# Kernel tuning notes

Hardware: AMD Instinct MI355X
Metric: run time of the kernel (lower is better)

The kernel has to match this reference:

```python
import jax, jax.numpy as jnp
import numpy as np

B, C_IN, C_OUT, N, T = 32, 64, 192, 307, 24
DILATIONS = (1, 2)
O3 = C_OUT // 3  # out channels per branch


def setup_inputs() -> dict:
    key = jax.random.key(0)
    ks = iter(jax.random.split(key, 32))
    nrm = lambda shape: 0.05 * jax.random.normal(next(ks), shape, dtype=jnp.float32)
    return {
        "x": jax.random.normal(next(ks), (B, C_IN, N, T), dtype=jnp.float32),
        "adj": jax.random.randint(next(ks), (N, N), 0, 2, dtype=jnp.int32),
        "ln_g": jnp.ones((T,), jnp.float32),
        "ln_b": jnp.zeros((T,), jnp.float32),
        "res_W": nrm((C_OUT, C_IN)), "res_b": nrm((C_OUT,)),
        "ca_W1": nrm((T,)), "ca_W2": nrm((N, T)), "ca_W3": nrm((N,)),
        "cc_W": nrm((O3, C_IN)), "cc_b": nrm((O3,)),
        "ta_W1": nrm((N,)), "ta_W2": nrm((C_IN, N)), "ta_W3": nrm((C_IN,)),
        "tc_W0": nrm((O3, C_IN, 1, 2)), "tc_b0": nrm((O3,)),
        "tc_W1": nrm((O3, O3, 1, 2)), "tc_b1": nrm((O3,)),
        "ga_W1": nrm((T,)), "ga_W2": nrm((C_IN, T)), "ga_W3": nrm((C_IN,)),
        "g_W": nrm((O3, C_IN)),
    }


def layer_norm_lastdim(x, g, b, eps=1e-5):
    mu = jnp.mean(x, axis=-1, keepdims=True)
    var = jnp.var(x, axis=-1, keepdims=True)
    return (x - mu) * jax.lax.rsqrt(var + eps) * g + b


def conv1x1(x, W, b):
    # x: [B,C,N,T], W: [O,C]
    return jnp.einsum("oc,bcnt->bont", W, x) + b[None, :, None, None]


def c_attention(x, W1, W2, W3):
    # channel attention over C; x: [B,C,N,T]
    lhs = jnp.einsum("bcn,nt->bct", jnp.einsum("bcnt,t->bcn", x, W1), W2)  # [B,C,T]
    rhs = jnp.einsum("n,bcnt->bct", W3, x)                                  # [B,C,T]
    att = jax.nn.softmax(jnp.einsum("bct,bdt->bcd", lhs, rhs), axis=-1)     # [B,C,C]
    return jnp.einsum("bcd,bdnt->bcnt", att, x)


def t_attention(x, W1, W2, W3):
    # temporal attention over T; x: [B,C,N,T]
    lhs = jnp.einsum("bct,cn->btn", jnp.einsum("bcnt,n->bct", x, W1), W2)   # [B,T,N]
    rhs = jnp.einsum("c,bcnt->bnt", W3, x)                                   # [B,N,T]
    att = jax.nn.softmax(jnp.einsum("btn,bns->bts", lhs, rhs), axis=-1)      # [B,T,T]
    return jnp.einsum("bts,bcns->bcnt", att, x)


def g_attention(x, adj, W1, W2, W3):
    # graph (spatial) attention over N, masked by adjacency; x: [B,C,N,T]
    lhs = jnp.einsum("bcn,ct->bnt", jnp.einsum("bcnt,t->bcn", x, W1), W2)   # [B,N,T]
    rhs = jnp.einsum("c,bcnt->bnt", W3, x)                                   # [B,N,T]
    scores = jnp.einsum("bnt,bmt->bnm", lhs, rhs)                            # [B,N,N]
    scores = jnp.where(adj[None] > 0, scores, jnp.float32(-1e30))
    att = jax.nn.softmax(scores, axis=-1)
    return jnp.einsum("bnm,bcmt->bcnt", att, x)


def causal_conv(x, W, b, d):
    # Conv2d kernel [1,2], dilation [1,d], pad [0,d] + Chomp(d) == left-pad-only causal conv
    y = jax.lax.conv_general_dilated(
        x, W, window_strides=(1, 1), padding=((0, 0), (d, 0)),
        rhs_dilation=(1, d), dimension_numbers=("NCHW", "OIHW", "NCHW"))
    return y + b[None, :, None, None]


def meam_forward(x, adj, ln_g, ln_b, res_W, res_b, ca_W1, ca_W2, ca_W3, cc_W, cc_b,
                 ta_W1, ta_W2, ta_W3, tc_W0, tc_b0, tc_W1, tc_b1,
                 ga_W1, ga_W2, ga_W3, g_W):
    h = layer_norm_lastdim(x, ln_g, ln_b)
    # CACN branch: channel attention + 1x1 conv
    c_out = conv1x1(c_attention(h, ca_W1, ca_W2, ca_W3), cc_W, cc_b)
    # TACN branch: temporal attention + dilated causal convs
    t_out = t_attention(h, ta_W1, ta_W2, ta_W3)
    t_out = causal_conv(t_out, tc_W0, tc_b0, DILATIONS[0])
    t_out = causal_conv(t_out, tc_W1, tc_b1, DILATIONS[1])
    # GACN branch: graph attention + channel mixing
    g_out = jnp.einsum("oc,bcnt->bont", g_W, g_attention(h, adj, ga_W1, ga_W2, ga_W3))
    out = jnp.concatenate([c_out, t_out, g_out], axis=1)  # [B, C_OUT, N, T]
    return jax.nn.relu(out + conv1x1(x, res_W, res_b))


def reference(x, adj, ln_g, ln_b, res_W, res_b, ca_W1, ca_W2, ca_W3, cc_W, cc_b,
              ta_W1, ta_W2, ta_W3, tc_W0, tc_b0, tc_W1, tc_b1,
              ga_W1, ga_W2, ga_W3, g_W):
    return meam_forward(x, adj, ln_g, ln_b, res_W, res_b, ca_W1, ca_W2, ca_W3, cc_W, cc_b,
                        ta_W1, ta_W2, ta_W3, tc_W0, tc_b0, tc_W1, tc_b1,
                        ga_W1, ga_W2, ga_W3, g_W)
```

## Files before the change

### kernel.cpp

```cpp
#include <hip/hip_runtime.h>
#include <hip/hip_bf16.h>

#define BB 32
#define CC 64
#define NN 307
#define TT 24
#define CO 192
#define NT (NN*TT)
#define GO 1536

using bf16 = __hip_bfloat16;
typedef __attribute__((ext_vector_type(8))) short bf16x8;
typedef __attribute__((ext_vector_type(4))) float f32x4;

#define OFF_ln_g   0
#define OFF_ln_b   24
#define OFF_res_W  48
#define OFF_res_b  12336
#define OFF_ca_W1  12528
#define OFF_ca_W2  12552
#define OFF_ca_W3  19920
#define OFF_cc_W   20227
#define OFF_cc_b   24323
#define OFF_ta_W1  24387
#define OFF_ta_W2  24694
#define OFF_ta_W3  44342
#define OFF_tc_W0  44406
#define OFF_tc_b0  52598
#define OFF_tc_W1  52662
#define OFF_tc_b1  60854
#define OFF_ga_W1  60918
#define OFF_ga_W2  60942
#define OFF_ga_W3  62478
#define OFF_g_W    62542
#define W_TOTAL    66638

__device__ __forceinline__ float xload(const void* p, size_t i, int f) {
  return f ? ((const float*)p)[i] : __bfloat162float(((const bf16*)p)[i]);
}
__device__ __forceinline__ void ostore(void* p, size_t i, float v, int f) {
  if (f) ((float*)p)[i] = v; else ((bf16*)p)[i] = __float2bfloat16(v);
}
__device__ __forceinline__ float oload(const void* p, size_t i, int f) {
  return f ? ((const float*)p)[i] : __bfloat162float(((const bf16*)p)[i]);
}

__global__ void MEAM_44787918963464_kernel() {}

__global__ __launch_bounds__(256) void k_probe(const void* lng_raw, int* flag) {
  if (threadIdx.x == 0 && blockIdx.x == 0) {
    unsigned w = *(const unsigned*)lng_raw;
    *flag = (w == 0x3F800000u) ? 1 : 0;
  }
}

__global__ __launch_bounds__(256) void k_cvt_w(
    const void* p0, const void* p1, const void* p2, const void* p3,
    const void* p4, const void* p5, const void* p6, const void* p7,
    const void* p8, const void* p9, const void* p10, const void* p11,
    const void* p12, const void* p13, const void* p14, const void* p15,
    const void* p16, const void* p17, const void* p18, const void* p19,
    const int* flagp, float* dst) {
  int i = blockIdx.x*256 + threadIdx.x;
  if (i >= W_TOTAL) return;
  const void* ps[20] = {p0,p1,p2,p3,p4,p5,p6,p7,p8,p9,p10,p11,p12,p13,p14,p15,p16,p17,p18,p19};
  const int sz[20] = {24,24,12288,192,24,7368,307,4096,64,307,19648,64,8192,64,8192,64,24,1536,64,4096};
  int f = *flagp;
  int s = 0, base = 0;
  while (i >= base + sz[s]) { base += sz[s]; s++; }
  dst[i] = f ? ((const float*)ps[s])[i-base]
             : __bfloat162float(((const bf16*)ps[s])[i-base]);
}

__global__ __launch_bounds__(256) void k_prep_tc(const float* __restrict__ W,
    bf16* __restrict__ Ag, float* __restrict__ tb_bias) {
  int g = blockIdx.x*256 + threadIdx.x;
  if (g >= CC*CC) return;
  int pI = g >> 6, c = g & 63;
  const float* W0 = W + OFF_tc_W0;
  const float* b0 = W + OFF_tc_b0;
  const float* W1 = W + OFF_tc_W1;
  const float* b1 = W + OFF_tc_b1;
  const float* resW = W + OFF_res_W;
  const float* resb = W + OFF_res_b;
  float m0=0.f,m1=0.f,m2=0.f,m3=0.f, bb0=0.f, bb2=0.f;
  for (int o=0;o<CC;o++){
    float a1v = W1[(pI*CC+o)*2], b1v = W1[(pI*CC+o)*2+1];
    float a0v = W0[(o*CC+c)*2],  b0v = W0[(o*CC+c)*2+1];
    m0 += b1v*b0v; m1 += b1v*a0v; m2 += a1v*b0v; m3 += a1v*a0v;
    bb0 += b1v*b0[o]; bb2 += a1v*b0[o];
  }
  Ag[pI*320 + 0*64 + c] = __float2bfloat16(m0);
  Ag[pI*320 + 1*64 + c] = __float2bfloat16(m1);
  Ag[pI*320 + 2*64 + c] = __float2bfloat16(m2);
  Ag[pI*320 + 3*64 + c] = __float2bfloat16(m3);
  Ag[pI*320 + 4*64 + c] = __float2bfloat16(resW[(64+pI)*CC + c]);
  if (c == 0){
    tb_bias[pI]    = b1[pI] + bb0 + resb[64+pI];
    tb_bias[64+pI] = bb2;
  }
}

__global__ __launch_bounds__(256) void k_prep_A(const float* __restrict__ Mc,
    const float* __restrict__ W, bf16* __restrict__ Apre) {
  int idx = blockIdx.x*256 + threadIdx.x;
  if (idx >= BB*192*128) return;
  int b = idx / 24576;
  int rem = idx - b*24576;
  int p2 = rem >> 7, k = rem & 127;
  const float* resW = W + OFF_res_W;
  const float* gW   = W + OFF_g_W;
  float v;
  if (p2 < 64)       v = (k < 64) ? Mc[b*CC*CC + p2*CC + k] : resW[p2*CC + (k-64)];
  else if (p2 < 128) v = (k < 64) ? gW[(p2-64)*CC + k] : 0.f;
  else               v = (k < 64) ? 0.f : resW[p2*CC + (k-64)];
  Apre[idx] = __float2bfloat16(v);
}

__global__ __launch_bounds__(256) void k_ln(const void* __restrict__ x, const int* flagp,
    const float* __restrict__ W,
    float* __restrict__ mu_o, float* __restrict__ rs_o,
    float* __restrict__ xw1c, float* __restrict__ xw1g) {
  int r = blockIdx.x*256 + threadIdx.x;
  if (r >= BB*CC*NN) return;
  int f = *flagp;
  const float* lng  = W + OFF_ln_g;
  const float* lnb  = W + OFF_ln_b;
  const float* caW1 = W + OFF_ca_W1;
  const float* gaW1 = W + OFF_ga_W1;
  float v[TT];
  float mu = 0.f;
  for (int t=0;t<TT;t++){ v[t] = xload(x, (size_t)r*TT+t, f); mu += v[t]; }
  mu *= (1.f/TT);
  float var = 0.f;
  for (int t=0;t<TT;t++){ float d=v[t]-mu; var += d*d; }
  var *= (1.f/TT);
  float rs = rsqrtf(var + 1e-5f);
  float s1=0.f, s2=0.f;
  for (int t=0;t<TT;t++){
    float hv = (v[t]-mu)*rs*lng[t] + lnb[t];
    s1 += hv*caW1[t];
    s2 += hv*gaW1[t];
  }
  mu_o[r]=mu; rs_o[r]=rs; xw1c[r]=s1; xw1g[r]=s2;
}

__global__ __launch_bounds__(256) void k_prep_ct(const void* __restrict__ x, const int* flagp,
    const float* __restrict__ mu_a, const float* __restrict__ rs_a,
    const float* __restrict__ W, const float* __restrict__ xw1c,
    float* __restrict__ lhsc, float* __restrict__ rhsc, float* __restrict__ xw1t) {
  int i = blockIdx.x*256 + threadIdx.x;
  if (i >= BB*CC*TT) return;
  int f = *flagp;
  const float* lng  = W + OFF_ln_g;
  const float* lnb  = W + OFF_ln_b;
  const float* caW2 = W + OFF_ca_W2;
  const float* caW3 = W + OFF_ca_W3;
  const float* taW1 = W + OFF_ta_W1;
  int t = i % TT; int bc = i / TT;
  float gt = lng[t], bt = lnb[t];
  float l=0.f, rr=0.f, xt=0.f;
  for (int n=0;n<NN;n++){
    int row = bc*NN + n;
    float hv = (xload(x, (size_t)row*TT+t, f) - mu_a[row]) * rs_a[row] * gt + bt;
    l  += xw1c[row]*caW2[n*TT+t];
    rr += caW3[n]*hv;
    xt += taW1[n]*hv;
  }
  lhsc[i]=l; rhsc[i]=rr; xw1t[i]=xt;
}

__global__ __launch_bounds__(256) void k_prep_bn(const void* __restrict__ x, const int* flagp,
    const float* __restrict__ mu_a, const float* __restrict__ rs_a,
    const float* __restrict__ W, const float* __restrict__ xw1g,
    float* __restrict__ rhst, float* __restrict__ rhsg, float* __restrict__ lhsg) {
  int i = blockIdx.x*256 + threadIdx.x;
  if (i >= BB*NN*TT) return;
  int f = *flagp;
  const float* lng  = W + OFF_ln_g;
  const float* lnb  = W + OFF_ln_b;
  const float* taW3 = W + OFF_ta_W3;
  const float* gaW3 = W + OFF_ga_W3;
  const float* gaW2 = W + OFF_ga_W2;
  int t = i % TT; int n = (i/TT)%NN; int b = i/(NN*TT);
  float gt = lng[t], bt = lnb[t];
  float a=0.f,c2=0.f,d=0.f;
  for (int c=0;c<CC;c++){
    int row = (b*CC+c)*NN + n;
    float hv = (xload(x, (size_t)row*TT+t, f) - mu_a[row]) * rs_a[row] * gt + bt;
    a  += taW3[c]*hv;
    c2 += gaW3[c]*hv;
    d  += xw1g[row]*gaW2[c*TT+t];
  }
  rhst[i]=a; rhsg[i]=c2; lhsg[i]=d;
}

__global__ __launch_bounds__(256) void k_lhs_t(const float* __restrict__ xw1t,
    const float* __restrict__ W, float* __restrict__ lhst) {
  int i = blockIdx.x*256 + threadIdx.x;
  if (i >= BB*TT*NN) return;
  const float* taW2 = W + OFF_ta_W2;
  int n = i % NN; int t = (i/NN)%TT; int b = i/(TT*NN);
  float acc=0.f;
  for (int c=0;c<CC;c++)
    acc += xw1t[(b*CC+c)*TT+t]*taW2[c*NN+n];
  lhst[i]=acc;
}

__global__ __launch_bounds__(256) void k_att_c(const float* __restrict__ lhsc,
    const float* __restrict__ rhsc, const float* __restrict__ W,
    float* __restrict__ Mc) {
  int b = blockIdx.x; int tid = threadIdx.x;
  const float* ccW = W + OFF_cc_W;
  __shared__ float lc[CC*TT], rc[CC*TT], sc[CC*(CC+1)];
  for (int e=tid;e<CC*TT;e+=256){
    lc[e]=lhsc[b*CC*TT+e];
    rc[e]=rhsc[b*CC*TT+e];
  }
  __syncthreads();
  for (int e=tid;e<CC*CC;e+=256){
    int c=e>>6, d=e&63; float s=0.f;
    for (int t=0;t<TT;t++) s += lc[c*TT+t]*rc[d*TT+t];
    sc[c*(CC+1)+d]=s;
  }
  __syncthreads();
  if (tid<CC){
    float mx=-1e30f;
    for (int d=0;d<CC;d++) mx=fmaxf(mx, sc[tid*(CC+1)+d]);
    float sum=0.f;
    for (int d=0;d<CC;d++){ float e2=__expf(sc[tid*(CC+1)+d]-mx); sc[tid*(CC+1)+d]=e2; sum+=e2; }
    float inv=1.f/sum;
    for (int d=0;d<CC;d++) sc[tid*(CC+1)+d]*=inv;
  }
  __syncthreads();
  for (int e=tid;e<CC*CC;e+=256){
    int o=e>>6, d=e&63; float acc=0.f;
    for (int c=0;c<CC;c++) acc += ccW[o*CC+c]*sc[c*(CC+1)+d];
    Mc[b*CC*CC+e]=acc;
  }
}

__global__ __launch_bounds__(256) void k_att_t(const float* __restrict__ lhst,
    const float* __restrict__ rhst, float* __restrict__ attt) {
  int b=blockIdx.x, tid=threadIdx.x;
  __shared__ float sc[TT*TT];
  for (int e=tid;e<TT*TT;e+=256){
    int t=e/TT, s=e%TT;
    float acc=0.f;
    for (int n=0;n<NN;n++)
      acc += lhst[(b*TT+t)*NN+n]*rhst[(b*NN+n)*TT+s];
    sc[e]=acc;
  }
  __syncthreads();
  if (tid < TT){
    float mx=-1e30f;
    for (int s=0;s<TT;s++) mx=fmaxf(mx,sc[tid*TT+s]);
    float sum=0.f;
    for (int s=0;s<TT;s++){ float e=__expf(sc[tid*TT+s]-mx); sc[tid*TT+s]=e; sum+=e; }
    float inv=1.f/sum;
    for (int s=0;s<TT;s++) attt[b*TT*TT + tid*TT + s]=sc[tid*TT+s]*inv;
  }
}

__global__ __launch_bounds__(256) void k_att_g(const float* __restrict__ lhsg,
    const float* __restrict__ rhsg, const int* __restrict__ adj,
    bf16* __restrict__ attgh) {
  int n = blockIdx.x, b = blockIdx.y, tid = threadIdx.x;
  __shared__ float ls[TT];
  __shared__ float sv[NN];
  __shared__ float red[256];
  if (tid < TT) ls[tid] = lhsg[(b*NN+n)*TT + tid];
  __syncthreads();
  float lmax = -1e30f;
  for (int m=tid;m<NN;m+=256){
    float s = -1e30f;
    if (adj[n*NN+m] > 0){
      const float* rr = rhsg + ((size_t)b*NN+m)*TT;
      float acc=0.f;
      for (int t=0;t<TT;t++) acc += ls[t]*rr[t];
      s = acc;
    }
    sv[m]=s; lmax=fmaxf(lmax,s);
  }
  red[tid]=lmax; __syncthreads();
  for (int k=128;k>0;k>>=1){ if (tid<k) red[tid]=fmaxf(red[tid],red[tid+k]); __syncthreads(); }
  float mx = red[0]; __syncthreads();
  float lsum=0.f;
  for (int m=tid;m<NN;m+=256){
    float e = (sv[m] > -1e29f) ? __expf(sv[m]-mx) : 0.f;
    sv[m]=e; lsum+=e;
  }
  red[tid]=lsum; __syncthreads();
  for (int k=128;k>0;k>>=1){ if (tid<k) red[tid]+=red[tid+k]; __syncthreads(); }
  float inv = 1.f/red[0];
  for (int m=tid;m<NN;m+=256)
    attgh[((size_t)b*NN+n)*NN+m] = __float2bfloat16(sv[m]*inv);
}

__global__ __launch_bounds__(256) void k_hgc_mfma(
    const void* __restrict__ x, const int* flagp,
    const float* __restrict__ mu_a, const float* __restrict__ rs_a,
    const float* __restrict__ W, const bf16* __restrict__ Apre,
    bf16* __restrict__ hg, void* __restrict__ out) {
  int jt = blockIdx.x, b = blockIdx.y, tid = threadIdx.x;
  int f = *flagp;
  int j0 = jt*64;
  const float* lng = W + OFF_ln_g;
  const float* lnb = W + OFF_ln_b;
  const float* ccb = W + OFF_cc_b;
  const float* resb= W + OFF_res_b;
  __shared__ unsigned short Bs[64*128];

  {
    int c = tid >> 2, jg = tid & 3;
    float xv[16];
    int jbase = j0 + jg*16;
    size_t xoff = (size_t)(b*CC + c)*NT + jbase;
    if (jbase + 15 < NT) {
      if (f) {
        const float4* xp = (const float4*)((const float*)x + xoff);
        #pragma unroll
        for (int v=0; v<4; v++){ float4 q = xp[v]; xv[v*4]=q.x; xv[v*4+1]=q.y; xv[v*4+2]=q.z; xv[v*4+3]=q.w; }
      } else {
        const uint4* xp = (const uint4*)((const unsigned short*)x + xoff);
        #pragma unroll
        for (int v=0; v<2; v++){
          uint4 q = xp[v]; unsigned u[4]={q.x,q.y,q.z,q.w};
          #pragma unroll
          for (int kk2=0;kk2<4;kk2++){
            union{unsigned uu;float fl;} lo,hi;
            lo.uu=u[kk2]<<16; hi.uu=u[kk2]&0xffff0000u;
            xv[v*8+kk2*2]=lo.fl; xv[v*8+kk2*2+1]=hi.fl;
          }
        }
      }
    } else {
      #pragma unroll
      for (int i=0;i<16;i++){ int j=jbase+i; xv[i] = (j<NT)? xload(x, xoff+i, f) : 0.f; }
    }
    const float* mu_r = mu_a + (b*CC+c)*NN;
    const float* rs_r = rs_a + (b*CC+c)*NN;
    #pragma unroll
    for (int i=0;i<16;i++){
      int j = jbase + i;
      int jl = jg*16 + i;
      float hv = 0.f, xf = 0.f;
      if (j < NT){
        int n = j / 24, t = j - n*24;
        xf = xv[i];
        hv = (xf - mu_r[n]) * rs_r[n] * lng[t] + lnb[t];
      }
      int cs = c ^ ((jl&7)<<3);
      bf16 hb = __float2bfloat16(hv), xb = __float2bfloat16(xf);
      Bs[jl*128 + cs]      = *(unsigned short*)&hb;
      Bs[jl*128 + cs + 64] = *(unsigned short*)&xb;
    }
  }

  int lane = tid & 63, w = tid >> 6;
  int q = lane >> 4, lr = lane & 15;
  bf16x8 afo[4], afh[2], afr[2];
  {
    const unsigned short* Ab = (const unsigned short*)Apre + (size_t)b*24576;
    const unsigned short* r0 = Ab + (w*16 + lr)*128;
    #pragma unroll
    for (int kc=0;kc<4;kc++) afo[kc] = *(const bf16x8*)&r0[kc*32 + q*8];
    const unsigned short* r1 = Ab + (64 + w*16 + lr)*128;
    #pragma unroll
    for (int kc=0;kc<2;kc++) afh[kc] = *(const bf16x8*)&r1[kc*32 + q*8];
    const unsigned short* r2 = Ab + (128 + w*16 + lr)*128;
    #pragma unroll
    for (int kc=0;kc<2;kc++) afr[kc] = *(const bf16x8*)&r2[(kc+2)*32 + q*8];
  }
  f32x4 z4 = {0.f,0.f,0.f,0.f};
  f32x4 acco[4] = {z4,z4,z4,z4};
  f32x4 acch[4] = {z4,z4,z4,z4};
  f32x4 accr[4] = {z4,z4,z4,z4};
  __syncthreads();

  #pragma unroll
  for (int ct=0; ct<4; ct++){
    int jl = ct*16 + lr;
    int sw = ((jl&7)<<3);
    #pragma unroll
    for (int kc=0; kc<4; kc++){
      int ke = (kc*32 + q*8) ^ sw;
      bf16x8 bfr = *(const bf16x8*)&Bs[jl*128 + ke];
      acco[ct] = __builtin_amdgcn_mfma_f32_16x16x32_bf16(afo[kc], bfr, acco[ct], 0,0,0);
      if (kc < 2)
        acch[ct] = __builtin_amdgcn_mfma_f32_16x16x32_bf16(afh[kc], bfr, acch[ct], 0,0,0);
      else
        accr[ct] = __builtin_amdgcn_mfma_f32_16x16x32_bf16(afr[kc-2], bfr, accr[ct], 0,0,0);
    }
  }

  #pragma unroll
  for (int ct=0;ct<4;ct++){
    int jl = ct*16 + lr;
    int j = j0 + jl;
    if (j < NT){
      #pragma unroll
      for (int r=0;r<4;r++){
        int p2 = w*16 + q*4 + r;
        float v = acco[ct][r] + ccb[p2] + resb[p2];
        ostore(out, ((size_t)b*CO + p2)*NT + j, fmaxf(v,0.f), f);
      }
      int n = j/24, t2 = j - n*24;
      size_t hb2 = ((size_t)b*NN + n)*GO + t2;
      #pragma unroll
      for (int r=0;r<4;r++){
        int o = w*16 + q*4 + r;
        hg[hb2 + o*TT] = __float2bfloat16(acch[ct][r]);
      }
      #pragma unroll
      for (int r=0;r<4;r++){
        int p3 = w*16 + q*4 + r;
        ostore(out, ((size_t)b*CO + 128 + p3)*NT + j, accr[ct][r] + resb[128+p3], f);
      }
    }
  }
}

__global__ __launch_bounds__(256) void k_gemm_g(const bf16* __restrict__ attgh,
    const bf16* __restrict__ hg, const int* flagp, void* __restrict__ out) {
  int jt = blockIdx.x, nt = blockIdx.y, b = blockIdx.z;
  int tid = threadIdx.x;
  int f = *flagp;
  int n0 = nt*64, j0 = jt*64;
  __shared__ unsigned short As[64*72];
  __shared__ unsigned short Bs[64*72];
  int lane = tid & 63, w = tid >> 6;
  int q = lane >> 4, lr = lane & 15;
  f32x4 z4 = {0.f,0.f,0.f,0.f};
  f32x4 acc[4] = {z4,z4,z4,z4};
  const unsigned short* Ag = (const unsigned short*)attgh + (size_t)b*NN*NN;
  const unsigned short* Bg = (const unsigned short*)hg + (size_t)b*NN*GO;
  for (int m0=0;m0<NN;m0+=64){
    for (int u=tid; u<512; u+=256){
      int r=u>>3, kb=(u&7)*8;
      int gn=n0+r, gm=m0+kb;
      if (gn<NN && gm+7<NN){
        *(uint4*)&As[r*72+kb] = *(const uint4*)&Ag[(size_t)gn*NN + gm];
      } else {
        for (int i2=0;i2<8;i2++){
          int m=gm+i2;
          As[r*72+kb+i2] = (gn<NN && m<NN) ? Ag[(size_t)gn*NN+m] : 0;
        }
      }
    }
    for (int u=tid; u<512; u+=256){
      int m=u>>3, jb=(u&7)*8;
      int gm=m0+m;
      if (gm<NN){
        unsigned short s[8];
        *(uint4*)s = *(const uint4*)&Bg[(size_t)gm*GO + j0 + jb];
        #pragma unroll
        for (int i2=0;i2<8;i2++) Bs[(jb+i2)*72 + m] = s[i2];
      } else {
        #pragma unroll
        for (int i2=0;i2<8;i2++) Bs[(jb+i2)*72 + m] = 0;
      }
    }
    __syncthreads();
    #pragma unroll
    for (int kk=0;kk<64;kk+=32){
      bf16x8 af = *(const bf16x8*)&As[(w*16+lr)*72 + kk + q*8];
      #pragma unroll
      for (int ct=0;ct<4;ct++){
        bf16x8 bfr = *(const bf16x8*)&Bs[(ct*16+lr)*72 + kk + q*8];
        acc[ct] = __builtin_amdgcn_mfma_f32_16x16x32_bf16(af, bfr, acc[ct], 0,0,0);
      }
    }
    __syncthreads();
  }
  #pragma unroll
  for (int ct=0;ct<4;ct++){
    #pragma unroll
    for (int r=0;r<4;r++){
      int n = n0 + w*16 + q*4 + r;
      if (n >= NN) continue;
      int j = j0 + ct*16 + lr;
      int o = j/TT, t2 = j%TT;
      size_t idx = ((size_t)b*CO + 128 + o)*NT + (size_t)n*TT + t2;
      float v = acc[ct][r] + oload(out, idx, f);
      ostore(out, idx, fmaxf(v, 0.f), f);
    }
  }
}

__global__ __launch_bounds__(256) void k_cmix(const float* __restrict__ Mc,
    const void* __restrict__ x, const int* flagp,
    const float* __restrict__ mu_a, const float* __restrict__ rs_a,
    const float* __restrict__ W, void* __restrict__ out) {
  int jt=blockIdx.x, b=blockIdx.y, tid=threadIdx.x;
  int f = *flagp;
  int j0=jt*64;
  const float* lng = W + OFF_ln_g;
  const float* lnb = W + OFF_ln_b;
  const float* ccb = W + OFF_cc_b;
  __shared__ float Ms[CC*64];
  __shared__ float Hs[CC*64];
  for (int e=tid;e<CC*64;e+=256){
    int o=e&63, d=e>>6;
    Ms[e]=Mc[b*CC*CC + o*CC + d];
  }
  for (int e=tid;e<CC*64;e+=256){
    int d=e>>6, j=e&63; int jj=j0+j;
    float hv = 0.f;
    if (jj<NT){
      int n = jj/TT, t = jj%TT;
      int row = (b*CC+d)*NN + n;
      hv = (xload(x, (size_t)(b*CC+d)*NT + jj, f) - mu_a[row]) * rs_a[row] * lng[t] + lnb[t];
    }
    Hs[e]=hv;
  }
  __syncthreads();
  int ti=tid&15, tj=tid>>4;
  float acc[4][4]={};
  for (int d=0;d<CC;d++){
    float4 a4=*(const float4*)&Ms[d*64+ti*4];
    float4 b4=*(const float4*)&Hs[d*64+tj*4];
    float av[4]={a4.x,a4.y,a4.z,a4.w};
    float bv[4]={b4.x,b4.y,b4.z,b4.w};
    for (int i=0;i<4;i++)
      for (int j=0;j<4;j++) acc[i][j]+=av[i]*bv[j];
  }
  for (int i=0;i<4;i++){
    int o=ti*4+i; float bias=ccb[o];
    for (int j=0;j<4;j++){
      int jj=j0+tj*4+j;
      if (jj<NT)
        ostore(out, ((size_t)b*CO+o)*NT+jj, acc[i][j]+bias, f);
    }
  }
}

__global__ __launch_bounds__(256) void k_graph(const float* __restrict__ lhsg,
    const float* __restrict__ rhsg, const int* __restrict__ adj,
    const void* __restrict__ x, const int* flagp,
    const float* __restrict__ mu_a, const float* __restrict__ rs_a,
    const float* __restrict__ W, void* __restrict__ out) {
  int n = blockIdx.x, b = blockIdx.y, tid = threadIdx.x;
  int f = *flagp;
  const float* lng = W + OFF_ln_g;
  const float* lnb = W + OFF_ln_b;
  const float* gW  = W + OFF_g_W;
  __shared__ float ls[TT];
  __shared__ float sv[NN];
  __shared__ float red[256];
  __shared__ float wl[NN];
  __shared__ int   ml[NN];
  __shared__ int   cnt;
  __shared__ float z[CC*TT];
  __shared__ float Gs[CC*CC];
  __shared__ float gs[TT], bs[TT];
  if (tid < TT){
    ls[tid] = lhsg[(b*NN+n)*TT + tid];
    gs[tid] = lng[tid]; bs[tid] = lnb[tid];
  }
  for (int e=tid;e<CC*CC;e+=256) Gs[e]=gW[e];
  __syncthreads();
  float lmax = -1e30f;
  for (int m=tid;m<NN;m+=256){
    float s = -1e30f;
    if (adj[n*NN+m] > 0){
      const float* rr = rhsg + ((size_t)b*NN+m)*TT;
      float acc=0.f;
      for (int t=0;t<TT;t++) acc += ls[t]*rr[t];
      s = acc;
    }
    sv[m]=s; lmax=fmaxf(lmax,s);
  }
  red[tid]=lmax; __syncthreads();
  for (int k=128;k>0;k>>=1){ if (tid<k) red[tid]=fmaxf(red[tid],red[tid+k]); __syncthreads(); }
  float mx = red[0]; __syncthreads();
  float lsum=0.f;
  for (int m=tid;m<NN;m+=256){
    float e = (sv[m] > -1e29f) ? __expf(sv[m]-mx) : 0.f;
    sv[m]=e; lsum+=e;
  }
  red[tid]=lsum; __syncthreads();
  for (int k=128;k>0;k>>=1){ if (tid<k) red[tid]+=red[tid+k]; __syncthreads(); }
  float inv = 1.f/red[0];
  if (tid==0){
    int c=0;
    for (int m=0;m<NN;m++) if (sv[m]!=0.f){ ml[c]=m; wl[c]=sv[m]*inv; c++; }
    cnt=c;
  }
  __syncthreads();
  int K = cnt;
  {
    int c = tid>>2, tg = tid&3;
    float acc[6]={0,0,0,0,0,0};
    float s0 = 0.f;
    const float* mu_r = mu_a + (b*CC+c)*NN;
    const float* rs_r = rs_a + (b*CC+c)*NN;
    size_t xbase = (size_t)(b*CC+c)*NT;
    for (int k=0;k<K;k++){
      int m = ml[k];
      float wr = wl[k]*rs_r[m];
      s0 += wr*mu_r[m];
      size_t xm = xbase + m*TT + tg*6;
      for (int j=0;j<6;j++) acc[j] += wr*xload(x, xm+j, f);
    }
    for (int j=0;j<6;j++){
      int t = tg*6+j;
      z[c*TT+t] = gs[t]*(acc[j]-s0) + bs[t];
    }
  }
  __syncthreads();
  {
    int o = tid>>2, tg = tid&3;
    float acc[6]={0,0,0,0,0,0};
    for (int c=0;c<CC;c++){
      float gwv = Gs[o*CC+c];
      const float* zr = &z[c*TT + tg*6];
      for (int j=0;j<6;j++) acc[j] += gwv*zr[j];
    }
    size_t base = ((size_t)b*CO + 128 + o)*NT + n*TT + tg*6;
    for (int j=0;j<6;j++)
      ostore(out, base+j, acc[j], f);
  }
}

__global__ __launch_bounds__(256) void k_tbranch(const void* __restrict__ x, const int* flagp,
    const float* __restrict__ mu_a, const float* __restrict__ rs_a,
    const float* __restrict__ W, const float* __restrict__ attt,
    void* __restrict__ out, int fuse) {
  int chunk = blockIdx.x, b = blockIdx.y, tid = threadIdx.x;
  int f = *flagp;
  int n0 = chunk*4;
  const float* lng = W + OFF_ln_g;
  const float* lnb = W + OFF_ln_b;
  const float* W0  = W + OFF_tc_W0;
  const float* b0  = W + OFF_tc_b0;
  const float* W1  = W + OFF_tc_W1;
  const float* b1  = W + OFF_tc_b1;
  __shared__ float hs[256*25];
  __shared__ float at[TT*TT];
  for (int e=tid;e<CC*4*TT;e+=256){
    int c=e/(4*TT), rem=e%(4*TT), i=rem/TT, t=rem%TT;
    int n=n0+i;
    float hv=0.f;
    if (n<NN){
      int row=(b*CC+c)*NN+n;
      hv = (xload(x,(size_t)row*TT+t,f) - mu_a[row]) * rs_a[row] * lng[t] + lnb[t];
    }
    hs[(c*4+i)*25+t] = hv;
  }
  for (int e=tid;e<TT*TT;e+=256) at[e]=attt[b*TT*TT+e];
  __syncthreads();
  {
    float r[TT], o2[TT];
    float* myrow = &hs[tid*25];
    #pragma unroll
    for (int s=0;s<TT;s++) r[s]=myrow[s];
    for (int t=0;t<TT;t++){
      float a=0.f;
      #pragma unroll
      for (int s=0;s<TT;s++) a += at[t*TT+s]*r[s];
      o2[t]=a;
    }
    #pragma unroll
    for (int t=0;t<TT;t++) myrow[t]=o2[t];
  }
  __syncthreads();
  {
    int o = tid>>2, i = tid&3;
    float acc[TT];
    float bb = b0[o];
    for (int t=0;t<TT;t++) acc[t]=bb;
    for (int c=0;c<CC;c++){
      float wa = W0[(o*CC+c)*2], wb = W0[(o*CC+c)*2+1];
      const float* row = &hs[(c*4+i)*25];
      acc[0] += wb*row[0];
      #pragma unroll
      for (int t=1;t<TT;t++) acc[t] += wa*row[t-1] + wb*row[t];
    }
    __syncthreads();
    float* myrow = &hs[tid*25];
    #pragma unroll
    for (int t=0;t<TT;t++) myrow[t]=acc[t];
  }
  __syncthreads();
  {
    int o2 = tid>>2, i = tid&3;
    int n = n0+i;
    float acc[TT];
    float bb = b1[o2];
    for (int t=0;t<TT;t++) acc[t]=bb;
    for (int o=0;o<CC;o++){
      float wa = W1[(o2*CC+o)*2], wb = W1[(o2*CC+o)*2+1];
      const float* row = &hs[(o*4+i)*25];
      acc[0] += wb*row[0];
      acc[1] += wb*row[1];
      #pragma unroll
      for (int t=2;t<TT;t++) acc[t] += wa*row[t-2] + wb*row[t];
    }
    if (n<NN){
      size_t base = (((size_t)b*CO + 64 + o2)*NN + n)*TT;
      if (fuse){
        for (int t=0;t<TT;t++){
          float v = acc[t] + oload(out, base+t, f);
          ostore(out, base+t, fmaxf(v,0.f), f);
        }
      } else {
        for (int t=0;t<TT;t++) ostore(out, base+t, acc[t], f);
      }
    }
  }
}

__device__ __forceinline__ void tb_load_raw(const void* __restrict__ x, int f, int b, int c, int nn,
    float* h) {
  if (nn < NN) {
    size_t off = (size_t)(b*CC + c)*NT + (size_t)nn*TT;
    if (f) {
      const float4* xp = (const float4*)((const float*)x + off);
      #pragma unroll
      for (int v=0; v<6; v++){
        float4 q = xp[v];
        h[v*4+0]=q.x; h[v*4+1]=q.y; h[v*4+2]=q.z; h[v*4+3]=q.w;
      }
    } else {
      const uint4* xp = (const uint4*)((const unsigned short*)x + off);
      #pragma unroll
      for (int v=0; v<3; v++){
        uint4 q = xp[v];
        unsigned wsv[4] = {q.x,q.y,q.z,q.w};
        #pragma unroll
        for (int k=0;k<4;k++){
          union { unsigned u; float fl; } lo, hi;
          lo.u = wsv[k] << 16; hi.u = wsv[k] & 0xffff0000u;
          h[v*8 + k*2] = lo.fl; h[v*8 + k*2 + 1] = hi.fl;
        }
      }
    }
  } else {
    #pragma unroll
    for (int t=0;t<TT;t++) h[t]=0.f;
  }
}

__global__ __launch_bounds__(256) void k_tb_mfma(
    const void* __restrict__ x, const int* flagp,
    const float* __restrict__ mu_a, const float* __restrict__ rs_a,
    const float* __restrict__ W, const float* __restrict__ attt,
    const bf16* __restrict__ Agm, const float* __restrict__ tb_bias,
    void* __restrict__ out) {
  int chunk = blockIdx.x, b = blockIdx.y, tid = threadIdx.x;
  int f = *flagp;
  int n0 = chunk*8;
  const float* lng = W + OFF_ln_g;
  const float* lnb = W + OFF_ln_b;
  __shared__ unsigned short Bs[8*27*64];
  __shared__ unsigned short Xs[8*24*64];

  for (int e=tid; e<8*3*64; e+=256){
    int n = e/192, rem = e%192, s = rem>>6, cz = rem&63;
    Bs[((n*27+s)<<6) + cz] = 0;
  }

  int c  = tid & 63;
  int nA = tid >> 6;
  float h0[TT], h1[TT];
  tb_load_raw(x, f, b, c, n0+nA,   h0);
  tb_load_raw(x, f, b, c, n0+nA+4, h1);
  #pragma unroll
  for (int t=0;t<TT;t++){
    int cs = c ^ ((t&7)<<3);
    bf16 v0 = __float2bfloat16(h0[t]);
    bf16 v1 = __float2bfloat16(h1[t]);
    Xs[(nA*24+t)*64 + cs]     = *reinterpret_cast<unsigned short*>(&v0);
    Xs[((nA+4)*24+t)*64 + cs] = *reinterpret_cast<unsigned short*>(&v1);
  }
  {
    int nn0 = n0+nA, nn1 = n0+nA+4;
    if (nn0 < NN){
      int r = (b*CC+c)*NN + nn0; float mu = mu_a[r], rs = rs_a[r];
      #pragma unroll
      for (int t=0;t<TT;t++) h0[t] = (h0[t]-mu)*rs*lng[t] + lnb[t];
    }
    if (nn1 < NN){
      int r = (b*CC+c)*NN + nn1; float mu = mu_a[r], rs = rs_a[r];
      #pragma unroll
      for (int t=0;t<TT;t++) h1[t] = (h1[t]-mu)*rs*lng[t] + lnb[t];
    }
  }
  const float* att_b = attt + b*TT*TT;
  for (int t=0;t<TT;t++){
    float a0=0.f, a1=0.f;
    #pragma unroll
    for (int s=0;s<TT;s++){
      float wv = att_b[t*TT+s];
      a0 += wv*h0[s]; a1 += wv*h1[s];
    }
    int sI = t+3;
    int cs = c ^ ((sI&7)<<3);
    bf16 v0 = __float2bfloat16(a0);
    bf16 v1 = __float2bfloat16(a1);
    Bs[((nA*27+sI)<<6) + cs]     = *reinterpret_cast<unsigned short*>(&v0);
    Bs[(((nA+4)*27+sI)<<6) + cs] = *reinterpret_cast<unsigned short*>(&v1);
  }

  int lane = tid & 63, w = tid >> 6;
  int q = lane >> 4, lr = lane & 15;
  bf16x8 af[10];
  const unsigned short* Arow = (const unsigned short*)Agm + (size_t)(w*16+lr)*320;
  #pragma unroll
  for (int kc=0;kc<10;kc++)
    af[kc] = *(const bf16x8*)&Arow[kc*32 + q*8];

  f32x4 z4 = {0.f,0.f,0.f,0.f};
  f32x4 acc[12] = {z4,z4,z4,z4,z4,z4,z4,z4,z4,z4,z4,z4};
  __syncthreads();

  #pragma unroll
  for (int ct=0; ct<12; ct++){
    int col = ct*16 + lr;
    int nl = col/24, t = col - nl*24;
    #pragma unroll
    for (int kc=0;kc<8;kc++){
      int tap = kc>>1;
      int s = t + 3 - tap;
      int cb = ((kc&1)*32 + q*8) ^ ((s&7)<<3);
      bf16x8 bfr = *(const bf16x8*)&Bs[((nl*27+s)<<6) + cb];
      acc[ct] = __builtin_amdgcn_mfma_f32_16x16x32_bf16(af[kc], bfr, acc[ct], 0,0,0);
    }
    #pragma unroll
    for (int kc2=0;kc2<2;kc2++){
      int cb = (kc2*32 + q*8) ^ ((t&7)<<3);
      bf16x8 bfr = *(const bf16x8*)&Xs[(nl*24+t)*64 + cb];
      acc[ct] = __builtin_amdgcn_mfma_f32_16x16x32_bf16(af[8+kc2], bfr, acc[ct], 0,0,0);
    }
  }

  #pragma unroll
  for (int ct=0;ct<12;ct++){
    int col = ct*16 + lr;
    int nl = col/24, t = col - nl*24;
    int nn = n0 + nl;
    if (nn < NN){
      #pragma unroll
      for (int r=0;r<4;r++){
        int pI = w*16 + q*4 + r;
        size_t idx = ((size_t)b*CO + 64 + pI)*NT + (size_t)nn*TT + t;
        float v = acc[ct][r] + tb_bias[pI] + (t>=2 ? tb_bias[64+pI] : 0.f);
        ostore(out, idx, fmaxf(v, 0.f), f);
      }
    }
  }
}

__global__ __launch_bounds__(256) void k_res_final(const void* __restrict__ x, const int* flagp,
    const float* __restrict__ W, void* __restrict__ out) {
  int jt=blockIdx.x, ot=blockIdx.y, b=blockIdx.z; int tid=threadIdx.x;
  int f = *flagp;
  int j0=jt*64, o0=ot*64;
  const float* resW = W + OFF_res_W;
  const float* resb = W + OFF_res_b;
  __shared__ float Ws[CC*64];
  __shared__ float Xs[CC*64];
  for (int e=tid;e<CC*64;e+=256){
    int o=e&63, c=e>>6;
    Ws[e] = resW[(o0+o)*CC + c];
  }
  for (int e=tid;e<CC*64;e+=256){
    int c=e>>6, j=e&63; int jj=j0+j;
    Xs[e] = (jj<NT) ? xload(x, (size_t)(b*CC+c)*NT + jj, f) : 0.f;
  }
  __syncthreads();
  int ti=tid&15, tj=tid>>4;
  float acc[4][4]={};
  for (int k=0;k<CC;k++){
    float4 a4=*(const float4*)&Ws[k*64+ti*4];
    float4 b4=*(const float4*)&Xs[k*64+tj*4];
    float av[4]={a4.x,a4.y,a4.z,a4.w};
    float bv[4]={b4.x,b4.y,b4.z,b4.w};
    for (int i=0;i<4;i++)
      for (int j=0;j<4;j++) acc[i][j]+=av[i]*bv[j];
  }
  for (int i=0;i<4;i++){
    int o=o0+ti*4+i; float bias=resb[o];
    for (int j=0;j<4;j++){
      int jj=j0+tj*4+j;
      if (jj<NT){
        size_t idx=((size_t)b*CO+o)*NT+jj;
        float v = acc[i][j] + bias + oload(out, idx, f);
        ostore(out, idx, fmaxf(v,0.f), f);
      }
    }
  }
}

extern "C" void kernel_launch(void* const* d_in, const int* in_sizes, int n_in,
                              void* d_out, int out_size, void* d_ws, size_t ws_size,
                              hipStream_t stream) {
  const void* x     = d_in[0];
  const int*  adj   = (const int*)d_in[1];
  void* out = d_out;

  float* p = (float*)d_ws;
  int*   flagp = (int*)p; p += 4;
  float* Wf  = p; p += W_TOTAL;
  float* mu_a = p; p += (size_t)BB*CC*NN;
  float* rs_a = p; p += (size_t)BB*CC*NN;
  float* xw1c = p; p += (size_t)BB*CC*NN;
  float* xw1g = p; p += (size_t)BB*CC*NN;
  float* xw1t = p; p += (size_t)BB*CC*TT;
  float* lhsc = p; p += (size_t)BB*CC*TT;
  float* rhsc = p; p += (size_t)BB*CC*TT;
  float* rhst = p; p += (size_t)BB*NN*TT;
  float* rhsg = p; p += (size_t)BB*NN*TT;
  float* lhsg = p; p += (size_t)BB*NN*TT;
  float* lhst = p; p += (size_t)BB*TT*NN;
  float* attt = p; p += (size_t)BB*TT*TT;
  float* Mc   = p; p += (size_t)BB*CC*CC;
  bf16*  Agm  = (bf16*)p; p += 10240;
  float* tb_bias = p; p += 128;
  bf16*  Apre = (bf16*)p; p += (size_t)BB*192*128/2;
  bf16*  attgh = (bf16*)p; p += (size_t)BB*NN*NN/2 + 16;
  bf16*  hg   = (bf16*)p;
  size_t need = ((char*)(hg + (size_t)BB*NN*GO)) - (char*)d_ws;
  bool gemm_path = (ws_size >= need);

  k_probe<<<dim3(1), dim3(256), 0, stream>>>(d_in[2], flagp);
  k_cvt_w<<<dim3((W_TOTAL+255)/256), dim3(256), 0, stream>>>(
      d_in[2], d_in[3], d_in[4], d_in[5], d_in[6], d_in[7], d_in[8], d_in[9],
      d_in[10], d_in[11], d_in[12], d_in[13], d_in[14], d_in[15], d_in[16],
      d_in[17], d_in[18], d_in[19], d_in[20], d_in[21], flagp, Wf);
  k_ln<<<dim3((BB*CC*NN+255)/256), dim3(256), 0, stream>>>(x, flagp, Wf, mu_a, rs_a, xw1c, xw1g);
  k_prep_ct<<<dim3((BB*CC*TT+255)/256), dim3(256), 0, stream>>>(x, flagp, mu_a, rs_a, Wf, xw1c, lhsc, rhsc, xw1t);
  k_prep_bn<<<dim3((BB*NN*TT+255)/256), dim3(256), 0, stream>>>(x, flagp, mu_a, rs_a, Wf, xw1g, rhst, rhsg, lhsg);
  k_lhs_t<<<dim3((BB*TT*NN+255)/256), dim3(256), 0, stream>>>(xw1t, Wf, lhst);
  k_att_c<<<dim3(BB), dim3(256), 0, stream>>>(lhsc, rhsc, Wf, Mc);
  k_att_t<<<dim3(BB), dim3(256), 0, stream>>>(lhst, rhst, attt);
  if (gemm_path) {
    k_prep_tc<<<dim3(16), dim3(256), 0, stream>>>(Wf, Agm, tb_bias);
    k_prep_A<<<dim3((BB*192*128+255)/256), dim3(256), 0, stream>>>(Mc, Wf, Apre);
    k_att_g<<<dim3(NN, BB), dim3(256), 0, stream>>>(lhsg, rhsg, adj, attgh);
    k_hgc_mfma<<<dim3((NT+63)/64, BB), dim3(256), 0, stream>>>(x, flagp, mu_a, rs_a, Wf, Apre, hg, out);
    k_tb_mfma<<<dim3((NN+7)/8, BB), dim3(256), 0, stream>>>(x, flagp, mu_a, rs_a, Wf, attt, Agm, tb_bias, out);
    k_gemm_g<<<dim3(GO/64, (NN+63)/64, BB), dim3(256), 0, stream>>>(attgh, hg, flagp, out);
  } else {
    k_cmix<<<dim3((NT+63)/64, BB), dim3(256), 0, stream>>>(Mc, x, flagp, mu_a, rs_a, Wf, out);
    k_graph<<<dim3(NN, BB), dim3(256), 0, stream>>>(lhsg, rhsg, adj, x, flagp, mu_a, rs_a, Wf, out);
    k_tbranch<<<dim3((NN+3)/4, BB), dim3(256), 0, stream>>>(x, flagp, mu_a, rs_a, Wf, attt, out, 0);
    k_res_final<<<dim3((NT+63)/64, 3, BB), dim3(256), 0, stream>>>(x, flagp, Wf, out);
  }
}
```

Measured before the change: 808.6 us.

## Compute graph attention scores via split-bf16 MFMA tiles and swizzle GEMM B tile

The per-row scalar graph score and softmax kernel is replaced by two kernels. The first computes 64x64 score tiles with MFMA, splitting each operand into high and low bf16 parts (three products) to keep near-fp32 accuracy, and writes masked fp32 scores to a new workspace buffer. The second runs a wave-per-row softmax using shuffle reductions. Separately, the shared-memory B tile in the graph GEMM gets an XOR swizzle to cut LDS bank conflicts on its transposed stores. The score path now pays an extra round trip of the fp32 score matrix through global memory.

```diff
diff --git a/kernel.cpp b/kernel.cpp
--- a/kernel.cpp
+++ b/kernel.cpp
@@ -262,39 +262,89 @@
   }
 }
 
-__global__ __launch_bounds__(256) void k_att_g(const float* __restrict__ lhsg,
+__global__ __launch_bounds__(256) void k_scores_g(const float* __restrict__ lhsg,
     const float* __restrict__ rhsg, const int* __restrict__ adj,
+    float* __restrict__ Sg) {
+  int mt = blockIdx.x, nt = blockIdx.y, b = blockIdx.z;
+  int n0 = nt*64, m0 = mt*64, tid = threadIdx.x;
+  __shared__ unsigned short Lh[64*40], Ll[64*40], Rh[64*40], Rl[64*40];
+  for (int e=tid; e<64*24; e+=256){
+    int r=e/24, t=e-(e/24)*24;
+    int gn=n0+r, gm=m0+r;
+    float lv = (gn<NN)? lhsg[((size_t)b*NN+gn)*TT+t] : 0.f;
+    float rv = (gm<NN)? rhsg[((size_t)b*NN+gm)*TT+t] : 0.f;
+    bf16 lh=__float2bfloat16(lv); float lhf=__bfloat162float(lh);
+    bf16 llo=__float2bfloat16(lv-lhf);
+    bf16 rh=__float2bfloat16(rv); float rhf=__bfloat162float(rh);
+    bf16 rlo=__float2bfloat16(rv-rhf);
+    Lh[r*40+t]=*(unsigned short*)&lh; Ll[r*40+t]=*(unsigned short*)&llo;
+    Rh[r*40+t]=*(unsigned short*)&rh; Rl[r*40+t]=*(unsigned short*)&rlo;
+  }
+  for (int e=tid; e<64*8; e+=256){
+    int r=e>>3, t=24+(e&7);
+    Lh[r*40+t]=0; Ll[r*40+t]=0; Rh[r*40+t]=0; Rl[r*40+t]=0;
+  }
+  __syncthreads();
+  int lane=tid&63, w=tid>>6, q=lane>>4, lr=lane&15;
+  bf16x8 ah = *(const bf16x8*)&Lh[(w*16+lr)*40 + q*8];
+  bf16x8 al = *(const bf16x8*)&Ll[(w*16+lr)*40 + q*8];
+  f32x4 z4={0.f,0.f,0.f,0.f};
+  f32x4 acc[4]={z4,z4,z4,z4};
+  #pragma unroll
+  for (int ct=0;ct<4;ct++){
+    bf16x8 bh = *(const bf16x8*)&Rh[(ct*16+lr)*40 + q*8];
+    bf16x8 bl = *(const bf16x8*)&Rl[(ct*16+lr)*40 + q*8];
+    acc[ct]=__builtin_amdgcn_mfma_f32_16x16x32_bf16(ah,bh,acc[ct],0,0,0);
+    acc[ct]=__builtin_amdgcn_mfma_f32_16x16x32_bf16(ah,bl,acc[ct],0,0,0);
+    acc[ct]=__builtin_amdgcn_mfma_f32_16x16x32_bf16(al,bh,acc[ct],0,0,0);
+  }
+  #pragma unroll
+  for (int ct=0;ct<4;ct++){
+    int m = m0 + ct*16 + lr;
+    #pragma unroll
+    for (int r=0;r<4;r++){
+      int n = n0 + w*16 + q*4 + r;
+      if (n<NN && m<NN){
+        float s = acc[ct][r];
+        if (adj[n*NN+m] <= 0) s = -1e30f;
+        Sg[((size_t)b*NN+n)*NN+m] = s;
+      }
+    }
+  }
+}
+
+__global__ __launch_bounds__(256) void k_smax_g(const float* __restrict__ Sg,
     bf16* __restrict__ attgh) {
-  int n = blockIdx.x, b = blockIdx.y, tid = threadIdx.x;
-  __shared__ float ls[TT];
-  __shared__ float sv[NN];
-  __shared__ float red[256];
-  if (tid < TT) ls[tid] = lhsg[(b*NN+n)*TT + tid];
-  __syncthreads();
-  float lmax = -1e30f;
-  for (int m=tid;m<NN;m+=256){
-    float s = -1e30f;
-    if (adj[n*NN+m] > 0){
-      const float* rr = rhsg + ((size_t)b*NN+m)*TT;
-      float acc=0.f;
-      for (int t=0;t<TT;t++) acc += ls[t]*rr[t];
-      s = acc;
-    }
-    sv[m]=s; lmax=fmaxf(lmax,s);
-  }
-  red[tid]=lmax; __syncthreads();
-  for (int k=128;k>0;k>>=1){ if (tid<k) red[tid]=fmaxf(red[tid],red[tid+k]); __syncthreads(); }
-  float mx = red[0]; __syncthreads();
-  float lsum=0.f;
-  for (int m=tid;m<NN;m+=256){
-    float e = (sv[m] > -1e29f) ? __expf(sv[m]-mx) : 0.f;
-    sv[m]=e; lsum+=e;
-  }
-  red[tid]=lsum; __syncthreads();
-  for (int k=128;k>0;k>>=1){ if (tid<k) red[tid]+=red[tid+k]; __syncthreads(); }
-  float inv = 1.f/red[0];
-  for (int m=tid;m<NN;m+=256)
-    attgh[((size_t)b*NN+n)*NN+m] = __float2bfloat16(sv[m]*inv);
+  int b = blockIdx.y;
+  int n = blockIdx.x*4 + (threadIdx.x>>6);
+  int lane = threadIdx.x & 63;
+  if (n >= NN) return;
+  const float* row = Sg + ((size_t)b*NN+n)*NN;
+  float v[5]; float mx = -1e30f;
+  #pragma unroll
+  for (int i=0;i<5;i++){
+    int m = lane + i*64;
+    v[i] = (m<NN)? row[m] : -1e30f;
+    mx = fmaxf(mx, v[i]);
+  }
+  #pragma unroll
+  for (int off=32; off; off>>=1) mx = fmaxf(mx, __shfl_xor(mx, off));
+  float sum = 0.f;
+  #pragma unroll
+  for (int i=0;i<5;i++){
+    int m = lane + i*64;
+    float e = (m<NN)? __expf(v[i]-mx) : 0.f;
+    v[i]=e; sum += e;
+  }
+  #pragma unroll
+  for (int off=32; off; off>>=1) sum += __shfl_xor(sum, off);
+  float inv = 1.f/sum;
+  bf16* orow = attgh + ((size_t)b*NN+n)*NN;
+  #pragma unroll
+  for (int i=0;i<5;i++){
+    int m = lane + i*64;
+    if (m<NN) orow[m] = __float2bfloat16(v[i]*inv);
+  }
 }
 
 __global__ __launch_bounds__(256) void k_hgc_mfma(
@@ -449,16 +499,21 @@
       }
     }
     for (int u=tid; u<512; u+=256){
-      int m=u>>3, jb=(u&7)*8;
-      int gm=m0+m;
-      if (gm<NN){
-        unsigned short s[8];
+      int m  = (u&7) | ((u>>6)<<3);
+      int jb = ((u>>3)&7)*8;
+      int gm = m0 + m;
+      unsigned short s[8];
+      if (gm < NN){
         *(uint4*)s = *(const uint4*)&Bg[(size_t)gm*GO + j0 + jb];
-        #pragma unroll
-        for (int i2=0;i2<8;i2++) Bs[(jb+i2)*72 + m] = s[i2];
       } else {
         #pragma unroll
-        for (int i2=0;i2<8;i2++) Bs[(jb+i2)*72 + m] = 0;
+        for (int i2=0;i2<8;i2++) s[i2]=0;
+      }
+      #pragma unroll
+      for (int i2=0;i2<8;i2++){
+        int j = jb + i2;
+        int col = ((((m>>3) ^ ((j>>3)&7)) << 3) | (m&7));
+        Bs[j*72 + col] = s[i2];
       }
     }
     __syncthreads();
@@ -467,7 +522,10 @@
       bf16x8 af = *(const bf16x8*)&As[(w*16+lr)*72 + kk + q*8];
       #pragma unroll
       for (int ct=0;ct<4;ct++){
-        bf16x8 bfr = *(const bf16x8*)&Bs[(ct*16+lr)*72 + kk + q*8];
+        int jrow = ct*16+lr;
+        int kb = kk + q*8;
+        int col = (((kb>>3) ^ ((jrow>>3)&7)) << 3);
+        bf16x8 bfr = *(const bf16x8*)&Bs[jrow*72 + col];
         acc[ct] = __builtin_amdgcn_mfma_f32_16x16x32_bf16(af, bfr, acc[ct], 0,0,0);
       }
     }
@@ -919,6 +977,7 @@
   bf16*  Agm  = (bf16*)p; p += 10240;
   float* tb_bias = p; p += 128;
   bf16*  Apre = (bf16*)p; p += (size_t)BB*192*128/2;
+  float* Sg   = p; p += (size_t)BB*NN*NN + 16;
   bf16*  attgh = (bf16*)p; p += (size_t)BB*NN*NN/2 + 16;
   bf16*  hg   = (bf16*)p;
   size_t need = ((char*)(hg + (size_t)BB*NN*GO)) - (char*)d_ws;
@@ -938,7 +997,9 @@
   if (gemm_path) {
     k_prep_tc<<<dim3(16), dim3(256), 0, stream>>>(Wf, Agm, tb_bias);
     k_prep_A<<<dim3((BB*192*128+255)/256), dim3(256), 0, stream>>>(Mc, Wf, Apre);
-    k_att_g<<<dim3(NN, BB), dim3(256), 0, stream>>>(lhsg, rhsg, adj, attgh);
+    int ntile = (NN+63)/64;
+    k_scores_g<<<dim3(ntile, ntile, BB), dim3(256), 0, stream>>>(lhsg, rhsg, adj, Sg);
+    k_smax_g<<<dim3((NN+3)/4, BB), dim3(256), 0, stream>>>(Sg, attgh);
     k_hgc_mfma<<<dim3((NT+63)/64, BB), dim3(256), 0, stream>>>(x, flagp, mu_a, rs_a, Wf, Apre, hg, out);
     k_tb_mfma<<<dim3((NN+7)/8, BB), dim3(256), 0, stream>>>(x, flagp, mu_a, rs_a, Wf, attt, Agm, tb_bias, out);
     k_gemm_g<<<dim3(GO/64, (NN+63)/64, BB), dim3(256), 0, stream>>>(attgh, hg, flagp, out);
```

Result: no change. 801.5 us (-0.9%).
